# Kernel optimization log

Measured on AMD Instinct MI355X. Metric: run time of the kernel, lower is better.

## Reference

```python
import jax, jax.numpy as jnp
import numpy as np

IMG = 64            # image_height = image_width = 64
NPTS = 300          # n_pts_per_ray
MIN_DEPTH, MAX_DEPTH = 0.1, 3.0
GRID = 16           # latent_dim -> 16^3 voxel grid
VOXEL_SIZE = 0.1
FOV_DEG = 60.0      # pytorch3d FoVPerspectiveCameras default
B = 8               # number of cameras / latents
EPS = 1e-10         # EmissionAbsorptionRaymarcher eps


def _look_at(eye, at):
    # pytorch3d look_at_view_transform: row-vector convention x_view = x_world @ R + T
    up = np.array([0.0, 1.0, 0.0])
    z = at - eye; z = z / np.linalg.norm(z)
    x = np.cross(up, z); x = x / np.linalg.norm(x)
    y = np.cross(z, x); y = y / np.linalg.norm(y)
    R = np.stack([x, y, z], axis=1)  # columns are camera axes
    T = -eye @ R
    return R, T


def setup_inputs():
    rng = np.random.default_rng(0)
    Rs, Ts = [], []
    for _ in range(B):
        eye = rng.standard_normal(3) * np.array([0.01, 0.0001, 0.01])
        at = rng.standard_normal(3) * 0.01
        R, T = _look_at(eye, at)
        Rs.append(R); Ts.append(T)

    def lin(fan_in, fan_out):
        bound = 1.0 / np.sqrt(fan_in)  # torch Linear default init
        W = rng.uniform(-bound, bound, size=(fan_in, fan_out))
        b = rng.uniform(-bound, bound, size=(fan_out,))
        return jnp.asarray(W, jnp.float32), jnp.asarray(b, jnp.float32)

    W1, b1 = lin(30, 60)
    W2, b2 = lin(60, 480)
    W3, b3 = lin(480, 4 * GRID ** 3)
    zs = jnp.asarray(rng.standard_normal((B, 30)), jnp.float32)
    return {"zs": zs, "W1": W1, "b1": b1, "W2": W2, "b2": b2, "W3": W3, "b3": b3,
            "R": jnp.asarray(np.stack(Rs), jnp.float32),
            "T": jnp.asarray(np.stack(Ts), jnp.float32)}


def _grid_sample3d(vol, xyz):
    # vol: (C, D, H, W); xyz: (..., 3) in [-1, 1]; trilinear, align_corners=True, zero padding
    C, D, H, W = vol.shape
    batch_shape = xyz.shape[:-1]
    p = xyz.reshape(-1, 3)
    ix = (p[:, 0] + 1.0) * 0.5 * (W - 1)
    iy = (p[:, 1] + 1.0) * 0.5 * (H - 1)
    iz = (p[:, 2] + 1.0) * 0.5 * (D - 1)
    x0 = jnp.floor(ix); y0 = jnp.floor(iy); z0 = jnp.floor(iz)
    tx = ix - x0; ty = iy - y0; tz = iz - z0
    out = jnp.zeros((C, p.shape[0]), vol.dtype)
    for dx, wx in ((0, 1.0 - tx), (1, tx)):
        for dy, wy in ((0, 1.0 - ty), (1, ty)):
            for dz, wz in ((0, 1.0 - tz), (1, tz)):
                xf, yf, zf = x0 + dx, y0 + dy, z0 + dz
                valid = ((xf >= 0) & (xf <= W - 1) & (yf >= 0) & (yf <= H - 1)
                         & (zf >= 0) & (zf <= D - 1))
                xi = jnp.clip(xf, 0, W - 1).astype(jnp.int32)
                yi = jnp.clip(yf, 0, H - 1).astype(jnp.int32)
                zi = jnp.clip(zf, 0, D - 1).astype(jnp.int32)
                w = jnp.where(valid, wx * wy * wz, 0.0)
                out = out + w[None, :] * vol[:, zi, yi, xi]
    return jnp.moveaxis(out.reshape((C,) + batch_shape), 0, -1)


def _forward(zs, W1, b1, W2, b2, W3, b3, R, T):
    # latent MLP -> (B, 4, 16, 16, 16) volume (1 density channel + 3 color channels)
    h = jax.nn.sigmoid(zs @ W1 + b1)
    h = jax.nn.sigmoid(h @ W2 + b2)
    lat = jax.nn.sigmoid(h @ W3 + b3).reshape(-1, 4, GRID, GRID, GRID)
    densities = lat[:, 0:1]   # (B,1,D,H,W)
    colors = lat[:, 1:4]      # (B,3,D,H,W)

    # NDCGridRaysampler pixel-center grid (pytorch3d NDC: +x left, +y up, row 0 at max y)
    half_pix = 1.0 / IMG
    xs = jnp.linspace(1.0 - half_pix, -1.0 + half_pix, IMG)
    ys = jnp.linspace(1.0 - half_pix, -1.0 + half_pix, IMG)
    f = 1.0 / jnp.tan(jnp.deg2rad(FOV_DEG) / 2.0)  # focal from fov, aspect=1
    dir_cam = jnp.stack([jnp.broadcast_to(xs[None, :] / f, (IMG, IMG)),
                         jnp.broadcast_to(ys[:, None] / f, (IMG, IMG)),
                         jnp.ones((IMG, IMG))], axis=-1)  # (H,W,3)
    Rt = jnp.swapaxes(R, 1, 2)                             # view->world rotation
    dirs_w = jnp.einsum('hwc,bcd->bhwd', dir_cam, Rt)      # (B,H,W,3)
    origins_w = jnp.einsum('bc,bcd->bd', -T, Rt)           # camera centers (B,3)

    depths = jnp.linspace(MIN_DEPTH, MAX_DEPTH, NPTS)
    pts = origins_w[:, None, None, None, :] + dirs_w[:, :, :, None, :] * depths[None, None, None, :, None]
    half_extent = (GRID - 1) * VOXEL_SIZE * 0.5            # pytorch3d Volumes world->local scale
    local = pts / half_extent                              # (B,H,W,P,3)

    sigma = jax.vmap(_grid_sample3d)(densities, local)[..., 0]  # (B,H,W,P)
    feats = jax.vmap(_grid_sample3d)(colors, local)             # (B,H,W,P,3)

    # EmissionAbsorptionRaymarcher (surface_thickness=1)
    a = (1.0 + EPS) - sigma
    cp = jnp.cumprod(a, axis=-1)
    absorption = jnp.concatenate([jnp.ones_like(cp[..., :1]), cp[..., :-1]], axis=-1)
    weights = sigma * absorption
    rgb = jnp.sum(weights[..., None] * feats, axis=-2)          # (B,H,W,3)
    opacity = 1.0 - jnp.prod(1.0 - sigma, axis=-1, keepdims=True)
    return jnp.concatenate([rgb, opacity], axis=-1)             # (B,H,W,4)


def reference(zs, W1, b1, W2, b2, W3, b3, R, T):
    imgs = _forward(zs, W1, b1, W2, b2, W3, b3, R, T)
    return imgs[..., 3:4], imgs[..., 0:3]
```

## Files before the change

### kernel.cpp

```cpp
#include <hip/hip_runtime.h>
#include <hip/hip_bf16.h>

#define IMG 64
#define NPTS 300
#define GRIDN 16
#define BATCH 8

typedef __hip_bfloat16 bf16;

__device__ __forceinline__ float sigm(float x) { return 1.0f / (1.0f + __expf(-x)); }
__device__ __forceinline__ float lo_bf(unsigned u) { return __uint_as_float(u << 16); }
__device__ __forceinline__ float hi_bf(unsigned u) { return __uint_as_float(u & 0xffff0000u); }
__device__ __forceinline__ float us_bf(unsigned short u) {
    return __uint_as_float(((unsigned)u) << 16);
}

template <typename T>
__device__ __forceinline__ float ldv(const void* p, int i);
template <>
__device__ __forceinline__ float ldv<float>(const void* p, int i) { return ((const float*)p)[i]; }
template <>
__device__ __forceinline__ float ldv<bf16>(const void* p, int i) {
    return __bfloat162float(((const bf16*)p)[i]);
}

__device__ __forceinline__ void sniff(const void* W1, int* sflag, int t) {
    if (t < 64) {
        float m = 0.0f;
        for (int i = t; i < 1800; i += 64) {
            float v = fabsf(__bfloat162float(((const bf16*)W1)[i]));
            if (!(v < 1e30f)) v = 1e30f;
            m = fmaxf(m, v);
        }
#pragma unroll
        for (int d = 1; d < 64; d <<= 1) m = fmaxf(m, __shfl_xor(m, d));
        if (t == 0) *sflag = (m > 4.0f) ? 1 : 0;
    }
}

template <typename T>
__device__ void prep_body(const void* zs, const void* b1, const void* W1, const void* W2,
                          const void* b2, const void* W3, float* __restrict__ partial) {
    __shared__ float z[BATCH][30];
    __shared__ float h1[BATCH][60];
    __shared__ float h2s[BATCH][30];
    int t = threadIdx.x;
    int jb = blockIdx.x;
    int s = blockIdx.y;
    int i0 = s * 30;

    if (t < 240) {
        int b = t / 30, i = t - b * 30;
        z[b][i] = ldv<T>(zs, t);
    }
    __syncthreads();
    for (int idx = t; idx < 480; idx += 256) {
        int b = idx / 60, j = idx - b * 60;
        float acc = ldv<T>(b1, j);
#pragma unroll
        for (int i = 0; i < 30; ++i) acc = fmaf(z[b][i], ldv<T>(W1, i * 60 + j), acc);
        h1[b][j] = sigm(acc);
    }
    __syncthreads();
    if (t < 240) {
        int b = t / 30, rr = t - b * 30;
        int col = i0 + rr;
        float acc = ldv<T>(b2, col);
#pragma unroll
        for (int i = 0; i < 60; ++i) acc = fmaf(h1[b][i], ldv<T>(W2, i * 480 + col), acc);
        h2s[b][rr] = sigm(acc);
    }
    __syncthreads();

    int j0 = jb * 1024 + t * 4;
    float acc[BATCH][4];
#pragma unroll
    for (int b = 0; b < BATCH; ++b)
#pragma unroll
        for (int c = 0; c < 4; ++c) acc[b][c] = 0.0f;

#pragma unroll 6
    for (int i = 0; i < 30; ++i) {
        float w0, w1, w2, w3v;
        if (sizeof(T) == 2) {
            ushort4 q = *(const ushort4*)((const unsigned short*)W3 + (size_t)(i0 + i) * 16384 + j0);
            w0 = us_bf(q.x); w1 = us_bf(q.y); w2 = us_bf(q.z); w3v = us_bf(q.w);
        } else {
            float4 q = *(const float4*)((const float*)W3 + (size_t)(i0 + i) * 16384 + j0);
            w0 = q.x; w1 = q.y; w2 = q.z; w3v = q.w;
        }
#pragma unroll
        for (int b = 0; b < BATCH; ++b) {
            float h = h2s[b][i];
            acc[b][0] = fmaf(h, w0, acc[b][0]);
            acc[b][1] = fmaf(h, w1, acc[b][1]);
            acc[b][2] = fmaf(h, w2, acc[b][2]);
            acc[b][3] = fmaf(h, w3v, acc[b][3]);
        }
    }
#pragma unroll
    for (int b = 0; b < BATCH; ++b) {
        float4 st = {acc[b][0], acc[b][1], acc[b][2], acc[b][3]};
        *(float4*)(partial + ((size_t)(s * BATCH + b) << 14) + j0) = st;
    }
}

__global__ __launch_bounds__(256) void prep_kernel(const void* zs, const void* W1,
                                                   const void* b1, const void* W2,
                                                   const void* b2, const void* W3,
                                                   float* __restrict__ partial,
                                                   int* __restrict__ flag) {
    __shared__ int sflag;
    int t = threadIdx.x;
    sniff(W1, &sflag, t);
    __syncthreads();
    if (blockIdx.x == 0 && blockIdx.y == 0 && t == 0) *flag = sflag;
    if (sflag)
        prep_body<float>(zs, b1, W1, W2, b2, W3, partial);
    else
        prep_body<bf16>(zs, b1, W1, W2, b2, W3, partial);
}

__global__ __launch_bounds__(256) void w3_reduce_kernel(const float* __restrict__ partial,
                                                        const void* b3, bf16* __restrict__ volbf,
                                                        const int* __restrict__ flag) {
    int tid = blockIdx.x * 256 + threadIdx.x;
    int b = tid >> 14, j = tid & 16383;
    float a = 0.0f;
#pragma unroll
    for (int s = 0; s < 16; ++s) a += partial[((size_t)(s * BATCH + b) << 14) + j];
    a += (*flag) ? ldv<float>(b3, j) : ldv<bf16>(b3, j);
    a = sigm(a);
    int c = j >> 12, v = j & 4095;
    volbf[(size_t)((b << 12) + v) * 4 + c] = __float2bfloat16(a);
}

__global__ __launch_bounds__(256) void render_kernel(const void* Rm, const void* Tm,
                                                     const bf16* __restrict__ volbf, void* out,
                                                     const int* __restrict__ flag) {
    __shared__ uint2 vox[4096];
    int t = threadIdx.x;
    int rayBase = blockIdx.x * 64;
    int b = rayBase >> 12;
    const uint2* src = (const uint2*)(volbf + (size_t)b * 4096 * 4);
    for (int i = t; i < 4096; i += 256) vox[i] = src[i];
    __syncthreads();

    int f32out = *flag;
    int ray = rayBase + (t >> 2);
    int seg = t & 3;
    int pix = ray & 4095;
    int h = pix >> 6, w = pix & 63;

    const float inv_f = 0.57735026919f;
    float dcx = (0.984375f - 0.03125f * (float)w) * inv_f;
    float dcy = (0.984375f - 0.03125f * (float)h) * inv_f;

    float R[9], Tv[3];
    if (f32out) {
#pragma unroll
        for (int i = 0; i < 9; ++i) R[i] = ((const float*)Rm)[b * 9 + i];
#pragma unroll
        for (int i = 0; i < 3; ++i) Tv[i] = ((const float*)Tm)[b * 3 + i];
    } else {
#pragma unroll
        for (int i = 0; i < 9; ++i) R[i] = __bfloat162float(((const bf16*)Rm)[b * 9 + i]);
#pragma unroll
        for (int i = 0; i < 3; ++i) Tv[i] = __bfloat162float(((const bf16*)Tm)[b * 3 + i]);
    }

    float dx_ = dcx * R[0] + dcy * R[1] + R[2];
    float dy_ = dcx * R[3] + dcy * R[4] + R[5];
    float dz_ = dcx * R[6] + dcy * R[7] + R[8];
    float ox = -(Tv[0] * R[0] + Tv[1] * R[1] + Tv[2] * R[2]);
    float oy = -(Tv[0] * R[3] + Tv[1] * R[4] + Tv[2] * R[5]);
    float oz = -(Tv[0] * R[6] + Tv[1] * R[7] + Tv[2] * R[8]);

    float tA = -1e30f, tB = 1e30f;
    bool miss = false;
    {
        float dd[3] = {dx_, dy_, dz_}, oo[3] = {ox, oy, oz};
#pragma unroll
        for (int a = 0; a < 3; ++a) {
            if (fabsf(dd[a]) > 1e-8f) {
                float inv = 1.0f / dd[a];
                float ra = (-0.85f - oo[a]) * inv, rb = (0.85f - oo[a]) * inv;
                tA = fmaxf(tA, fminf(ra, rb));
                tB = fminf(tB, fmaxf(ra, rb));
            } else if (fabsf(oo[a]) >= 0.85f) {
                miss = true;
            }
        }
    }
    const float step = 2.9f / 299.0f;
    const float inv_step = 299.0f / 2.9f;
    int ilo = 0, ihi = -1;
    if (!miss && tB > tA) {
        float flo = fmaxf(-2.0f, fminf(302.0f, ceilf((tA - 0.1f) * inv_step)));
        float fhi = fmaxf(-2.0f, fminf(302.0f, floorf((tB - 0.1f) * inv_step)));
        ilo = (int)flo - 1;
        ihi = (int)fhi + 1;
        if (ilo < 0) ilo = 0;
        if (ihi > 299) ihi = 299;
    }
    int n = ihi - ilo + 1;
    if (n < 0) n = 0;
    int s0 = ilo + (n * seg) / 4;
    int s1 = ilo + (n * (seg + 1)) / 4;

    float cr = 0.f, cg = 0.f, cb = 0.f, Pa = 1.f;
    for (int i = s0; i < s1; ++i) {
        float tt = 0.1f + step * (float)i;
        float ix = fmaf(fmaf(tt, dx_, ox), 10.0f, 7.5f);
        float iy = fmaf(fmaf(tt, dy_, oy), 10.0f, 7.5f);
        float iz = fmaf(fmaf(tt, dz_, oz), 10.0f, 7.5f);
        float fx = floorf(ix), fy = floorf(iy), fz = floorf(iz);
        float txf = ix - fx, tyf = iy - fy, tzf = iz - fz;
        int x0 = (int)fx, y0 = (int)fy, z0 = (int)fz;
        float wx0 = (x0 >= 0 && x0 <= 15) ? (1.0f - txf) : 0.0f;
        float wx1 = (x0 >= -1 && x0 <= 14) ? txf : 0.0f;
        float wy0 = (y0 >= 0 && y0 <= 15) ? (1.0f - tyf) : 0.0f;
        float wy1 = (y0 >= -1 && y0 <= 14) ? tyf : 0.0f;
        float wz0 = (z0 >= 0 && z0 <= 15) ? (1.0f - tzf) : 0.0f;
        float wz1 = (z0 >= -1 && z0 <= 14) ? tzf : 0.0f;
        int xi0 = min(max(x0, 0), 15), xi1 = min(max(x0 + 1, 0), 15);
        int yi0 = min(max(y0, 0), 15), yi1 = min(max(y0 + 1, 0), 15);
        int zi0 = min(max(z0, 0), 15), zi1 = min(max(z0 + 1, 0), 15);

        float sx = 0.f, sr = 0.f, sg = 0.f, sb = 0.f;
#define CORN(W, ZI, YI, XI)                              \
    {                                                    \
        uint2 q = vox[((ZI) << 8) + ((YI) << 4) + (XI)]; \
        sx = fmaf((W), lo_bf(q.x), sx);                  \
        sr = fmaf((W), hi_bf(q.x), sr);                  \
        sg = fmaf((W), lo_bf(q.y), sg);                  \
        sb = fmaf((W), hi_bf(q.y), sb);                  \
    }
        float wxy00 = wx0 * wy0, wxy10 = wx1 * wy0, wxy01 = wx0 * wy1, wxy11 = wx1 * wy1;
        CORN(wxy00 * wz0, zi0, yi0, xi0)
        CORN(wxy10 * wz0, zi0, yi0, xi1)
        CORN(wxy01 * wz0, zi0, yi1, xi0)
        CORN(wxy11 * wz0, zi0, yi1, xi1)
        CORN(wxy00 * wz1, zi1, yi0, xi0)
        CORN(wxy10 * wz1, zi1, yi0, xi1)
        CORN(wxy01 * wz1, zi1, yi1, xi0)
        CORN(wxy11 * wz1, zi1, yi1, xi1)
#undef CORN

        float wgt = sx * Pa;
        cr = fmaf(wgt, sr, cr);
        cg = fmaf(wgt, sg, cg);
        cb = fmaf(wgt, sb, cb);
        Pa *= (1.0f - sx);
    }

#pragma unroll
    for (int d = 1; d < 4; d <<= 1) {
        float o_cr = __shfl_xor(cr, d);
        float o_cg = __shfl_xor(cg, d);
        float o_cb = __shfl_xor(cb, d);
        float o_Pa = __shfl_xor(Pa, d);
        bool first = ((seg & d) == 0);
        cr = first ? fmaf(Pa, o_cr, cr) : fmaf(o_Pa, cr, o_cr);
        cg = first ? fmaf(Pa, o_cg, cg) : fmaf(o_Pa, cg, o_cg);
        cb = first ? fmaf(Pa, o_cb, cb) : fmaf(o_Pa, cb, o_cb);
        Pa *= o_Pa;
    }

    if (seg == 0) {
        if (f32out) {
            float* of = (float*)out;
            of[ray] = 1.0f - Pa;
            float* orgb = of + BATCH * IMG * IMG;
            orgb[ray * 3 + 0] = cr;
            orgb[ray * 3 + 1] = cg;
            orgb[ray * 3 + 2] = cb;
        } else {
            bf16* ob = (bf16*)out;
            ob[ray] = __float2bfloat16(1.0f - Pa);
            bf16* orgb = ob + BATCH * IMG * IMG;
            orgb[ray * 3 + 0] = __float2bfloat16(cr);
            orgb[ray * 3 + 1] = __float2bfloat16(cg);
            orgb[ray * 3 + 2] = __float2bfloat16(cb);
        }
    }
}

extern "C" void kernel_launch(void* const* d_in, const int* in_sizes, int n_in,
                              void* d_out, int out_size, void* d_ws, size_t ws_size,
                              hipStream_t stream) {
    const void* zs = d_in[0];
    const void* W1 = d_in[1];
    const void* b1 = d_in[2];
    const void* W2 = d_in[3];
    const void* b2 = d_in[4];
    const void* W3 = d_in[5];
    const void* b3 = d_in[6];
    const void* Rm = d_in[7];
    const void* Tm = d_in[8];

    bf16* volbf = (bf16*)d_ws;
    float* partial = (float*)((char*)d_ws + 262144);
    int* flag = (int*)((char*)d_ws + 262144 + (size_t)16 * BATCH * 16384 * 4);

    hipLaunchKernelGGL(prep_kernel, dim3(16, 16), dim3(256), 0, stream, zs, W1, b1, W2, b2, W3,
                       partial, flag);
    hipLaunchKernelGGL(w3_reduce_kernel, dim3(512), dim3(256), 0, stream, partial, b3, volbf,
                       flag);
    hipLaunchKernelGGL(render_kernel, dim3(512), dim3(256), 0, stream, Rm, Tm, volbf, d_out,
                       flag);
}
```

Baseline: 124.2 us.

## Fuse W3 reduction into prep kernel and add interior fast path for trilinear sampling

The split-K W3 matmul and its separate reduction kernel are replaced by one kernel. Each 512-thread block recomputes the full h2 activations (8x480) in shared memory and then computes the full 480-long dot product for 64 output columns across all 8 batches, applying bias and sigmoid directly. This removes a kernel launch and the partial-sum round trip through global memory, but every block redundantly recomputes layers 1-2 and the W3 reads become scalar per thread. The render loop also gains a fast path for samples whose 8 corners are all inside the grid, which skips the clamping and boundary-weight selection.

Result: slower. 141.0 us (+13.5%).

```diff
diff --git a/kernel.cpp b/kernel.cpp
--- a/kernel.cpp
+++ b/kernel.cpp
@@ -11,9 +11,6 @@
 __device__ __forceinline__ float sigm(float x) { return 1.0f / (1.0f + __expf(-x)); }
 __device__ __forceinline__ float lo_bf(unsigned u) { return __uint_as_float(u << 16); }
 __device__ __forceinline__ float hi_bf(unsigned u) { return __uint_as_float(u & 0xffff0000u); }
-__device__ __forceinline__ float us_bf(unsigned short u) {
-    return __uint_as_float(((unsigned)u) << 16);
-}
 
 template <typename T>
 __device__ __forceinline__ float ldv(const void* p, int i);
@@ -40,99 +37,70 @@
 
 template <typename T>
 __device__ void prep_body(const void* zs, const void* b1, const void* W1, const void* W2,
-                          const void* b2, const void* W3, float* __restrict__ partial) {
+                          const void* b2, const void* W3, const void* b3,
+                          bf16* __restrict__ volbf) {
     __shared__ float z[BATCH][30];
     __shared__ float h1[BATCH][60];
-    __shared__ float h2s[BATCH][30];
+    __shared__ __align__(16) float h2[BATCH][480];
     int t = threadIdx.x;
-    int jb = blockIdx.x;
-    int s = blockIdx.y;
-    int i0 = s * 30;
 
     if (t < 240) {
         int b = t / 30, i = t - b * 30;
         z[b][i] = ldv<T>(zs, t);
     }
     __syncthreads();
-    for (int idx = t; idx < 480; idx += 256) {
-        int b = idx / 60, j = idx - b * 60;
+    if (t < 480) {
+        int b = t / 60, j = t - b * 60;
         float acc = ldv<T>(b1, j);
 #pragma unroll
         for (int i = 0; i < 30; ++i) acc = fmaf(z[b][i], ldv<T>(W1, i * 60 + j), acc);
         h1[b][j] = sigm(acc);
     }
     __syncthreads();
-    if (t < 240) {
-        int b = t / 30, rr = t - b * 30;
-        int col = i0 + rr;
+    for (int idx = t; idx < BATCH * 480; idx += 512) {
+        int b = idx / 480, col = idx - b * 480;
         float acc = ldv<T>(b2, col);
 #pragma unroll
         for (int i = 0; i < 60; ++i) acc = fmaf(h1[b][i], ldv<T>(W2, i * 480 + col), acc);
-        h2s[b][rr] = sigm(acc);
-    }
-    __syncthreads();
-
-    int j0 = jb * 1024 + t * 4;
-    float acc[BATCH][4];
-#pragma unroll
-    for (int b = 0; b < BATCH; ++b)
-#pragma unroll
-        for (int c = 0; c < 4; ++c) acc[b][c] = 0.0f;
-
-#pragma unroll 6
-    for (int i = 0; i < 30; ++i) {
-        float w0, w1, w2, w3v;
-        if (sizeof(T) == 2) {
-            ushort4 q = *(const ushort4*)((const unsigned short*)W3 + (size_t)(i0 + i) * 16384 + j0);
-            w0 = us_bf(q.x); w1 = us_bf(q.y); w2 = us_bf(q.z); w3v = us_bf(q.w);
-        } else {
-            float4 q = *(const float4*)((const float*)W3 + (size_t)(i0 + i) * 16384 + j0);
-            w0 = q.x; w1 = q.y; w2 = q.z; w3v = q.w;
-        }
-#pragma unroll
-        for (int b = 0; b < BATCH; ++b) {
-            float h = h2s[b][i];
-            acc[b][0] = fmaf(h, w0, acc[b][0]);
-            acc[b][1] = fmaf(h, w1, acc[b][1]);
-            acc[b][2] = fmaf(h, w2, acc[b][2]);
-            acc[b][3] = fmaf(h, w3v, acc[b][3]);
-        }
-    }
-#pragma unroll
-    for (int b = 0; b < BATCH; ++b) {
-        float4 st = {acc[b][0], acc[b][1], acc[b][2], acc[b][3]};
-        *(float4*)(partial + ((size_t)(s * BATCH + b) << 14) + j0) = st;
-    }
-}
-
-__global__ __launch_bounds__(256) void prep_kernel(const void* zs, const void* W1,
+        h2[b][col] = sigm(acc);
+    }
+    __syncthreads();
+
+    int b = t >> 6;
+    int j = blockIdx.x * 64 + (t & 63);
+    float acc = ldv<T>(b3, j);
+#pragma unroll 2
+    for (int i = 0; i < 480; i += 8) {
+        float4 ha = *(const float4*)&h2[b][i];
+        float4 hb = *(const float4*)&h2[b][i + 4];
+        acc = fmaf(ha.x, ldv<T>(W3, (size_t)(i + 0) * 16384 + j), acc);
+        acc = fmaf(ha.y, ldv<T>(W3, (size_t)(i + 1) * 16384 + j), acc);
+        acc = fmaf(ha.z, ldv<T>(W3, (size_t)(i + 2) * 16384 + j), acc);
+        acc = fmaf(ha.w, ldv<T>(W3, (size_t)(i + 3) * 16384 + j), acc);
+        acc = fmaf(hb.x, ldv<T>(W3, (size_t)(i + 4) * 16384 + j), acc);
+        acc = fmaf(hb.y, ldv<T>(W3, (size_t)(i + 5) * 16384 + j), acc);
+        acc = fmaf(hb.z, ldv<T>(W3, (size_t)(i + 6) * 16384 + j), acc);
+        acc = fmaf(hb.w, ldv<T>(W3, (size_t)(i + 7) * 16384 + j), acc);
+    }
+    float a = sigm(acc);
+    int c = j >> 12, v = j & 4095;
+    volbf[(size_t)(((b << 12) + v) << 2) + c] = __float2bfloat16(a);
+}
+
+__global__ __launch_bounds__(512) void prep_kernel(const void* zs, const void* W1,
                                                    const void* b1, const void* W2,
                                                    const void* b2, const void* W3,
-                                                   float* __restrict__ partial,
+                                                   const void* b3, bf16* __restrict__ volbf,
                                                    int* __restrict__ flag) {
     __shared__ int sflag;
     int t = threadIdx.x;
     sniff(W1, &sflag, t);
     __syncthreads();
-    if (blockIdx.x == 0 && blockIdx.y == 0 && t == 0) *flag = sflag;
+    if (blockIdx.x == 0 && t == 0) *flag = sflag;
     if (sflag)
-        prep_body<float>(zs, b1, W1, W2, b2, W3, partial);
+        prep_body<float>(zs, b1, W1, W2, b2, W3, b3, volbf);
     else
-        prep_body<bf16>(zs, b1, W1, W2, b2, W3, partial);
-}
-
-__global__ __launch_bounds__(256) void w3_reduce_kernel(const float* __restrict__ partial,
-                                                        const void* b3, bf16* __restrict__ volbf,
-                                                        const int* __restrict__ flag) {
-    int tid = blockIdx.x * 256 + threadIdx.x;
-    int b = tid >> 14, j = tid & 16383;
-    float a = 0.0f;
-#pragma unroll
-    for (int s = 0; s < 16; ++s) a += partial[((size_t)(s * BATCH + b) << 14) + j];
-    a += (*flag) ? ldv<float>(b3, j) : ldv<bf16>(b3, j);
-    a = sigm(a);
-    int c = j >> 12, v = j & 4095;
-    volbf[(size_t)((b << 12) + v) * 4 + c] = __float2bfloat16(a);
+        prep_body<bf16>(zs, b1, W1, W2, b2, W3, b3, volbf);
 }
 
 __global__ __launch_bounds__(256) void render_kernel(const void* Rm, const void* Tm,
@@ -217,17 +185,40 @@
         float fx = floorf(ix), fy = floorf(iy), fz = floorf(iz);
         float txf = ix - fx, tyf = iy - fy, tzf = iz - fz;
         int x0 = (int)fx, y0 = (int)fy, z0 = (int)fz;
-        float wx0 = (x0 >= 0 && x0 <= 15) ? (1.0f - txf) : 0.0f;
-        float wx1 = (x0 >= -1 && x0 <= 14) ? txf : 0.0f;
-        float wy0 = (y0 >= 0 && y0 <= 15) ? (1.0f - tyf) : 0.0f;
-        float wy1 = (y0 >= -1 && y0 <= 14) ? tyf : 0.0f;
-        float wz0 = (z0 >= 0 && z0 <= 15) ? (1.0f - tzf) : 0.0f;
-        float wz1 = (z0 >= -1 && z0 <= 14) ? tzf : 0.0f;
-        int xi0 = min(max(x0, 0), 15), xi1 = min(max(x0 + 1, 0), 15);
-        int yi0 = min(max(y0, 0), 15), yi1 = min(max(y0 + 1, 0), 15);
-        int zi0 = min(max(z0, 0), 15), zi1 = min(max(z0 + 1, 0), 15);
 
         float sx = 0.f, sr = 0.f, sg = 0.f, sb = 0.f;
+        if (((unsigned)x0 < 15u) & ((unsigned)y0 < 15u) & ((unsigned)z0 < 15u)) {
+            int base = (z0 << 8) + (y0 << 4) + x0;
+            float wx0 = 1.0f - txf, wy0 = 1.0f - tyf, wz0 = 1.0f - tzf;
+            float wxy00 = wx0 * wy0, wxy10 = txf * wy0, wxy01 = wx0 * tyf, wxy11 = txf * tyf;
+#define CORNF(W, OFF)                          \
+    {                                          \
+        uint2 q = vox[base + (OFF)];           \
+        float wgt_ = (W);                      \
+        sx = fmaf(wgt_, lo_bf(q.x), sx);       \
+        sr = fmaf(wgt_, hi_bf(q.x), sr);       \
+        sg = fmaf(wgt_, lo_bf(q.y), sg);       \
+        sb = fmaf(wgt_, hi_bf(q.y), sb);       \
+    }
+            CORNF(wxy00 * wz0, 0)
+            CORNF(wxy10 * wz0, 1)
+            CORNF(wxy01 * wz0, 16)
+            CORNF(wxy11 * wz0, 17)
+            CORNF(wxy00 * tzf, 256)
+            CORNF(wxy10 * tzf, 257)
+            CORNF(wxy01 * tzf, 272)
+            CORNF(wxy11 * tzf, 273)
+#undef CORNF
+        } else {
+            float wx0 = (x0 >= 0 && x0 <= 15) ? (1.0f - txf) : 0.0f;
+            float wx1 = (x0 >= -1 && x0 <= 14) ? txf : 0.0f;
+            float wy0 = (y0 >= 0 && y0 <= 15) ? (1.0f - tyf) : 0.0f;
+            float wy1 = (y0 >= -1 && y0 <= 14) ? tyf : 0.0f;
+            float wz0 = (z0 >= 0 && z0 <= 15) ? (1.0f - tzf) : 0.0f;
+            float wz1 = (z0 >= -1 && z0 <= 14) ? tzf : 0.0f;
+            int xi0 = min(max(x0, 0), 15), xi1 = min(max(x0 + 1, 0), 15);
+            int yi0 = min(max(y0, 0), 15), yi1 = min(max(y0 + 1, 0), 15);
+            int zi0 = min(max(z0, 0), 15), zi1 = min(max(z0 + 1, 0), 15);
 #define CORN(W, ZI, YI, XI)                              \
     {                                                    \
         uint2 q = vox[((ZI) << 8) + ((YI) << 4) + (XI)]; \
@@ -236,16 +227,17 @@
         sg = fmaf((W), lo_bf(q.y), sg);                  \
         sb = fmaf((W), hi_bf(q.y), sb);                  \
     }
-        float wxy00 = wx0 * wy0, wxy10 = wx1 * wy0, wxy01 = wx0 * wy1, wxy11 = wx1 * wy1;
-        CORN(wxy00 * wz0, zi0, yi0, xi0)
-        CORN(wxy10 * wz0, zi0, yi0, xi1)
-        CORN(wxy01 * wz0, zi0, yi1, xi0)
-        CORN(wxy11 * wz0, zi0, yi1, xi1)
-        CORN(wxy00 * wz1, zi1, yi0, xi0)
-        CORN(wxy10 * wz1, zi1, yi0, xi1)
-        CORN(wxy01 * wz1, zi1, yi1, xi0)
-        CORN(wxy11 * wz1, zi1, yi1, xi1)
+            float wxy00 = wx0 * wy0, wxy10 = wx1 * wy0, wxy01 = wx0 * wy1, wxy11 = wx1 * wy1;
+            CORN(wxy00 * wz0, zi0, yi0, xi0)
+            CORN(wxy10 * wz0, zi0, yi0, xi1)
+            CORN(wxy01 * wz0, zi0, yi1, xi0)
+            CORN(wxy11 * wz0, zi0, yi1, xi1)
+            CORN(wxy00 * wz1, zi1, yi0, xi0)
+            CORN(wxy10 * wz1, zi1, yi0, xi1)
+            CORN(wxy01 * wz1, zi1, yi1, xi0)
+            CORN(wxy11 * wz1, zi1, yi1, xi1)
 #undef CORN
+        }
 
         float wgt = sx * Pa;
         cr = fmaf(wgt, sr, cr);
@@ -300,13 +292,10 @@
     const void* Tm = d_in[8];
 
     bf16* volbf = (bf16*)d_ws;
-    float* partial = (float*)((char*)d_ws + 262144);
-    int* flag = (int*)((char*)d_ws + 262144 + (size_t)16 * BATCH * 16384 * 4);
-
-    hipLaunchKernelGGL(prep_kernel, dim3(16, 16), dim3(256), 0, stream, zs, W1, b1, W2, b2, W3,
-                       partial, flag);
-    hipLaunchKernelGGL(w3_reduce_kernel, dim3(512), dim3(256), 0, stream, partial, b3, volbf,
-                       flag);
+    int* flag = (int*)((char*)d_ws + 262144);
+
+    hipLaunchKernelGGL(prep_kernel, dim3(256), dim3(512), 0, stream, zs, W1, b1, W2, b2, W3,
+                       b3, volbf, flag);
     hipLaunchKernelGGL(render_kernel, dim3(512), dim3(256), 0, stream, Rm, Tm, volbf, d_out,
                        flag);
 }
```

## Split W3 GEMV across more K slices and use padded voxel tile

Applied to the files above, without the earlier changes.

The prep kernel now splits the 480-row W3 reduction into 32 slices of 15 rows and uses 512-thread blocks where each half handles four batch entries, giving more blocks and fewer accumulators per thread. The reduce kernel sums 32 partials instead of 16. The render kernel stores the voxel grid in a zero-padded 20x20x20 shared tile, which removes per-corner bounds checks and clamps in the trilinear loop. In exchange, the partial buffer doubles in size, the reduce step reads twice as much, and shared memory per render block roughly doubles, which may lower occupancy.

After: 124.7 us. About the same (+0.4%).

```diff
diff --git a/kernel.cpp b/kernel.cpp
--- a/kernel.cpp
+++ b/kernel.cpp
@@ -5,6 +5,8 @@
 #define NPTS 300
 #define GRIDN 16
 #define BATCH 8
+#define KSLICES 32
+#define KROWS 15
 
 typedef __hip_bfloat16 bf16;
 
@@ -43,27 +45,27 @@
                           const void* b2, const void* W3, float* __restrict__ partial) {
     __shared__ float z[BATCH][30];
     __shared__ float h1[BATCH][60];
-    __shared__ float h2s[BATCH][30];
+    __shared__ float h2s[BATCH][KROWS];
     int t = threadIdx.x;
     int jb = blockIdx.x;
     int s = blockIdx.y;
-    int i0 = s * 30;
+    int i0 = s * KROWS;
 
     if (t < 240) {
         int b = t / 30, i = t - b * 30;
         z[b][i] = ldv<T>(zs, t);
     }
     __syncthreads();
-    for (int idx = t; idx < 480; idx += 256) {
-        int b = idx / 60, j = idx - b * 60;
+    if (t < 480) {
+        int b = t / 60, j = t - b * 60;
         float acc = ldv<T>(b1, j);
 #pragma unroll
         for (int i = 0; i < 30; ++i) acc = fmaf(z[b][i], ldv<T>(W1, i * 60 + j), acc);
         h1[b][j] = sigm(acc);
     }
     __syncthreads();
-    if (t < 240) {
-        int b = t / 30, rr = t - b * 30;
+    if (t < BATCH * KROWS) {
+        int b = t / KROWS, rr = t - b * KROWS;
         int col = i0 + rr;
         float acc = ldv<T>(b2, col);
 #pragma unroll
@@ -72,15 +74,17 @@
     }
     __syncthreads();
 
-    int j0 = jb * 1024 + t * 4;
-    float acc[BATCH][4];
-#pragma unroll
-    for (int b = 0; b < BATCH; ++b)
+    int th = t & 255;
+    int bh = t >> 8;
+    int j0 = jb * 1024 + th * 4;
+    float acc[4][4];
+#pragma unroll
+    for (int b = 0; b < 4; ++b)
 #pragma unroll
         for (int c = 0; c < 4; ++c) acc[b][c] = 0.0f;
 
-#pragma unroll 6
-    for (int i = 0; i < 30; ++i) {
+#pragma unroll
+    for (int i = 0; i < KROWS; ++i) {
         float w0, w1, w2, w3v;
         if (sizeof(T) == 2) {
             ushort4 q = *(const ushort4*)((const unsigned short*)W3 + (size_t)(i0 + i) * 16384 + j0);
@@ -90,8 +94,8 @@
             w0 = q.x; w1 = q.y; w2 = q.z; w3v = q.w;
         }
 #pragma unroll
-        for (int b = 0; b < BATCH; ++b) {
-            float h = h2s[b][i];
+        for (int b = 0; b < 4; ++b) {
+            float h = h2s[bh * 4 + b][i];
             acc[b][0] = fmaf(h, w0, acc[b][0]);
             acc[b][1] = fmaf(h, w1, acc[b][1]);
             acc[b][2] = fmaf(h, w2, acc[b][2]);
@@ -99,13 +103,13 @@
         }
     }
 #pragma unroll
-    for (int b = 0; b < BATCH; ++b) {
+    for (int b = 0; b < 4; ++b) {
         float4 st = {acc[b][0], acc[b][1], acc[b][2], acc[b][3]};
-        *(float4*)(partial + ((size_t)(s * BATCH + b) << 14) + j0) = st;
-    }
-}
-
-__global__ __launch_bounds__(256) void prep_kernel(const void* zs, const void* W1,
+        *(float4*)(partial + ((size_t)(s * BATCH + bh * 4 + b) << 14) + j0) = st;
+    }
+}
+
+__global__ __launch_bounds__(512) void prep_kernel(const void* zs, const void* W1,
                                                    const void* b1, const void* W2,
                                                    const void* b2, const void* W3,
                                                    float* __restrict__ partial,
@@ -128,7 +132,7 @@
     int b = tid >> 14, j = tid & 16383;
     float a = 0.0f;
 #pragma unroll
-    for (int s = 0; s < 16; ++s) a += partial[((size_t)(s * BATCH + b) << 14) + j];
+    for (int s = 0; s < KSLICES; ++s) a += partial[((size_t)(s * BATCH + b) << 14) + j];
     a += (*flag) ? ldv<float>(b3, j) : ldv<bf16>(b3, j);
     a = sigm(a);
     int c = j >> 12, v = j & 4095;
@@ -138,12 +142,17 @@
 __global__ __launch_bounds__(256) void render_kernel(const void* Rm, const void* Tm,
                                                      const bf16* __restrict__ volbf, void* out,
                                                      const int* __restrict__ flag) {
-    __shared__ uint2 vox[4096];
+    __shared__ uint2 vox[8000];
     int t = threadIdx.x;
     int rayBase = blockIdx.x * 64;
     int b = rayBase >> 12;
     const uint2* src = (const uint2*)(volbf + (size_t)b * 4096 * 4);
-    for (int i = t; i < 4096; i += 256) vox[i] = src[i];
+    for (int i = t; i < 8000; i += 256) vox[i] = make_uint2(0u, 0u);
+    __syncthreads();
+    for (int i = t; i < 4096; i += 256) {
+        int x = i & 15, y = (i >> 4) & 15, zc = i >> 8;
+        vox[(zc + 2) * 400 + (y + 2) * 20 + (x + 2)] = src[i];
+    }
     __syncthreads();
 
     int f32out = *flag;
@@ -217,35 +226,30 @@
         float fx = floorf(ix), fy = floorf(iy), fz = floorf(iz);
         float txf = ix - fx, tyf = iy - fy, tzf = iz - fz;
         int x0 = (int)fx, y0 = (int)fy, z0 = (int)fz;
-        float wx0 = (x0 >= 0 && x0 <= 15) ? (1.0f - txf) : 0.0f;
-        float wx1 = (x0 >= -1 && x0 <= 14) ? txf : 0.0f;
-        float wy0 = (y0 >= 0 && y0 <= 15) ? (1.0f - tyf) : 0.0f;
-        float wy1 = (y0 >= -1 && y0 <= 14) ? tyf : 0.0f;
-        float wz0 = (z0 >= 0 && z0 <= 15) ? (1.0f - tzf) : 0.0f;
-        float wz1 = (z0 >= -1 && z0 <= 14) ? tzf : 0.0f;
-        int xi0 = min(max(x0, 0), 15), xi1 = min(max(x0 + 1, 0), 15);
-        int yi0 = min(max(y0, 0), 15), yi1 = min(max(y0 + 1, 0), 15);
-        int zi0 = min(max(z0, 0), 15), zi1 = min(max(z0 + 1, 0), 15);
+
+        int base = z0 * 400 + y0 * 20 + x0 + 842;
+        float wx0 = 1.0f - txf, wy0 = 1.0f - tyf, wz0 = 1.0f - tzf;
+        float wxy00 = wx0 * wy0, wxy10 = txf * wy0, wxy01 = wx0 * tyf, wxy11 = txf * tyf;
 
         float sx = 0.f, sr = 0.f, sg = 0.f, sb = 0.f;
-#define CORN(W, ZI, YI, XI)                              \
-    {                                                    \
-        uint2 q = vox[((ZI) << 8) + ((YI) << 4) + (XI)]; \
-        sx = fmaf((W), lo_bf(q.x), sx);                  \
-        sr = fmaf((W), hi_bf(q.x), sr);                  \
-        sg = fmaf((W), lo_bf(q.y), sg);                  \
-        sb = fmaf((W), hi_bf(q.y), sb);                  \
-    }
-        float wxy00 = wx0 * wy0, wxy10 = wx1 * wy0, wxy01 = wx0 * wy1, wxy11 = wx1 * wy1;
-        CORN(wxy00 * wz0, zi0, yi0, xi0)
-        CORN(wxy10 * wz0, zi0, yi0, xi1)
-        CORN(wxy01 * wz0, zi0, yi1, xi0)
-        CORN(wxy11 * wz0, zi0, yi1, xi1)
-        CORN(wxy00 * wz1, zi1, yi0, xi0)
-        CORN(wxy10 * wz1, zi1, yi0, xi1)
-        CORN(wxy01 * wz1, zi1, yi1, xi0)
-        CORN(wxy11 * wz1, zi1, yi1, xi1)
-#undef CORN
+#define CORNP(W, OFF)                          \
+    {                                          \
+        uint2 q = vox[base + (OFF)];           \
+        float wgt_ = (W);                      \
+        sx = fmaf(wgt_, lo_bf(q.x), sx);       \
+        sr = fmaf(wgt_, hi_bf(q.x), sr);       \
+        sg = fmaf(wgt_, lo_bf(q.y), sg);       \
+        sb = fmaf(wgt_, hi_bf(q.y), sb);       \
+    }
+        CORNP(wxy00 * wz0, 0)
+        CORNP(wxy10 * wz0, 1)
+        CORNP(wxy01 * wz0, 20)
+        CORNP(wxy11 * wz0, 21)
+        CORNP(wxy00 * tzf, 400)
+        CORNP(wxy10 * tzf, 401)
+        CORNP(wxy01 * tzf, 420)
+        CORNP(wxy11 * tzf, 421)
+#undef CORNP
 
         float wgt = sx * Pa;
         cr = fmaf(wgt, sr, cr);
@@ -301,10 +305,10 @@
 
     bf16* volbf = (bf16*)d_ws;
     float* partial = (float*)((char*)d_ws + 262144);
-    int* flag = (int*)((char*)d_ws + 262144 + (size_t)16 * BATCH * 16384 * 4);
-
-    hipLaunchKernelGGL(prep_kernel, dim3(16, 16), dim3(256), 0, stream, zs, W1, b1, W2, b2, W3,
-                       partial, flag);
+    int* flag = (int*)((char*)d_ws + 262144 + (size_t)KSLICES * BATCH * 16384 * 4);
+
+    hipLaunchKernelGGL(prep_kernel, dim3(16, KSLICES), dim3(512), 0, stream, zs, W1, b1, W2,
+                       b2, W3, partial, flag);
     hipLaunchKernelGGL(w3_reduce_kernel, dim3(512), dim3(256), 0, stream, partial, b3, volbf,
                        flag);
     hipLaunchKernelGGL(render_kernel, dim3(512), dim3(256), 0, stream, Rm, Tm, volbf, d_out,
```
